# Kernel tuning notes

Measured on AMD Instinct MI355X. Metric: run time of the kernel, lower is better.

The kernel has to match this reference:

```python
import jax, jax.numpy as jnp
import numpy as np
from jax import lax

B, C, H = 64, 3, 224
F = 8  # number of 3x3 filters
POOL = (H - 2) // 2  # 111
FEAT = POOL * POOL * F  # 98568


def setup_inputs() -> dict:
    key = jax.random.key(0)
    ks = jax.random.split(key, 8)
    return {
        "x": jax.random.normal(ks[0], (B, C, H, H), dtype=jnp.float32),
        "filters": jax.random.normal(ks[1], (F, 3, 3), dtype=jnp.float32),
        "W1": jax.random.normal(ks[2], (FEAT, 512), dtype=jnp.float32) * 0.01,
        "b1": jax.random.normal(ks[3], (512,), dtype=jnp.float32) * 0.01,
        "W2": jax.random.normal(ks[4], (512, 256), dtype=jnp.float32) * 0.02,
        "b2": jax.random.normal(ks[5], (256,), dtype=jnp.float32) * 0.02,
        "Wo": jax.random.normal(ks[6], (256, 1000), dtype=jnp.float32) * 0.02,
        "bo": jax.random.normal(ks[7], (1000,), dtype=jnp.float32) * 0.02,
    }


def reference(x, filters, W1, b1, W2, b2, Wo, bo):
    # conv_r + conv_g + conv_b == conv(r+g+b, filt) by linearity -> sum channels once
    s = x.sum(axis=1, keepdims=True)  # [B,1,H,H]
    k = filters[:, None, :, :]  # [F,1,3,3] (OIHW)
    conv = lax.conv_general_dilated(
        s, k, window_strides=(1, 1), padding="VALID",
        dimension_numbers=("NCHW", "OIHW", "NCHW"))  # [B,F,222,222]
    conv = jax.nn.relu(conv)
    pooled = lax.reduce_window(
        conv, -jnp.inf, lax.max,
        window_dimensions=(1, 1, 2, 2), window_strides=(1, 1, 2, 2),
        padding="VALID")  # [B,F,111,111]
    flat = pooled.reshape(x.shape[0], -1)  # filter-major layout matches torch cat order
    h = jax.nn.relu(flat @ W1 + b1)
    h = jax.nn.relu(h @ W2 + b2)
    return jax.nn.softmax(h @ Wo + bo, axis=1)
```

## Files before the change

### kernel.cpp

```cpp
#include <hip/hip_runtime.h>
#include <math.h>

#define Bsz 64
#define Himg 224
#define HS (Himg*Himg)
#define PW 111
#define PP (PW*PW)
#define Fn 8
#define FEAT (Fn*PP)
#define FEATP 98592
#define KC 32
#define NT32_TOT 3081
#define NCH 192
#define N1 512
#define N2 256
#define N3 1000
#define RG 8

typedef short short8 __attribute__((ext_vector_type(8)));
typedef float f32x4 __attribute__((ext_vector_type(4)));

#define GLOAD_LDS16(g, l)                                                     \
  __builtin_amdgcn_global_load_lds(                                           \
      (const __attribute__((address_space(1))) void*)(g),                     \
      (__attribute__((address_space(3))) void*)(l), 16, 0, 0)

__device__ __forceinline__ void cvt_hilo(const float* v, short8& hi, short8& lo) {
#pragma unroll
  for (int j = 0; j < 8; j++) {
    unsigned u = __builtin_bit_cast(unsigned, v[j]);
    hi[j] = (short)(u >> 16);
    float hf = __builtin_bit_cast(float, u & 0xFFFF0000u);
    float r = v[j] - hf;
    lo[j] = (short)(__builtin_bit_cast(unsigned, r) >> 16);
  }
}

__device__ __forceinline__ unsigned packhl(float f) {
  unsigned u = __builtin_bit_cast(unsigned, f);
  unsigned hi = u >> 16;
  float hf = __builtin_bit_cast(float, u & 0xFFFF0000u);
  float r = f - hf;
  unsigned lo = __builtin_bit_cast(unsigned, r) >> 16;
  return (hi << 16) | (lo & 0xFFFFu);
}

__device__ __forceinline__ uint4 pack4(float4 f) {
  uint4 o;
  o.x = packhl(f.x); o.y = packhl(f.y); o.z = packhl(f.z); o.w = packhl(f.w);
  return o;
}

__global__ void k_convpool(const float* __restrict__ x, const float* __restrict__ filt,
                           float* __restrict__ flat) {
  int i = blockIdx.x * 256 + threadIdx.x;
  if (i < Bsz * (FEATP - FEAT))
    flat[(size_t)(i / 24) * FEATP + FEAT + (i % 24)] = 0.f;
  if (i >= Bsz * PP) return;
  int b = i / PP, r = i - b * PP;
  int py = r / PW, px = r - py * PW;
  const float* xb = x + (size_t)b * 3 * HS + (size_t)(2 * py) * Himg + 2 * px;
  float p[4][4];
#pragma unroll
  for (int dy = 0; dy < 4; dy++) {
    const float* row = xb + dy * Himg;
    float2 a0 = *(const float2*)(row);
    float2 a1 = *(const float2*)(row + 2);
    float2 b0 = *(const float2*)(row + HS);
    float2 b1 = *(const float2*)(row + HS + 2);
    float2 c0 = *(const float2*)(row + 2 * HS);
    float2 c1 = *(const float2*)(row + 2 * HS + 2);
    p[dy][0] = a0.x + b0.x + c0.x;
    p[dy][1] = a0.y + b0.y + c0.y;
    p[dy][2] = a1.x + b1.x + c1.x;
    p[dy][3] = a1.y + b1.y + c1.y;
  }
  float* outb = flat + (size_t)b * FEATP + r;
#pragma unroll
  for (int f = 0; f < Fn; f++) {
    float mx = 0.f;
#pragma unroll
    for (int oy = 0; oy < 2; oy++)
#pragma unroll
      for (int ox = 0; ox < 2; ox++) {
        float c = 0.f;
#pragma unroll
        for (int dy = 0; dy < 3; dy++)
#pragma unroll
          for (int dx = 0; dx < 3; dx++)
            c = fmaf(p[oy + dy][ox + dx], filt[f * 9 + dy * 3 + dx], c);
        mx = fmaxf(mx, c);
      }
    outb[(size_t)f * PP] = mx;
  }
}

__global__ void __launch_bounds__(256) k_gemm1(const float* __restrict__ A,
                                               const float* __restrict__ W,
                                               float* __restrict__ partial) {
  __shared__ float Wl[2][KC][128];
  __shared__ unsigned As[2][64 * 32];
  const int t = threadIdx.x;
  const int wv = t >> 6;
  const int lane = t & 63;
  const int wgid = blockIdx.x;
  const int nid = (wgid & 7) * 96 + (wgid >> 3);
  const int col0b = (nid & 3) * 128;
  const int c = nid >> 2;
  const int tile0 = c * 16 + min(c, 9);
  const int nt = (c < 9) ? 17 : 16;
  const int lrow = lane & 15;
  const int lg8 = (lane >> 4) * 8;
  const int gr = lg8 >> 2;
  const int sr = wv * 16 + (lane >> 3);
  const int sq = lane & 7;
  const int sgs = ((sq ^ (sr & 7)) << 2);
  const float* Ast = A + (size_t)sr * FEATP + sq * 4;
  const int wsr = lane >> 5;
  const int wscx = ((lane & 31) * 4) ^ ((wv & 1) << 4);
  const int wcol = wv * 32 + lrow;
  const int wcolsw = wcol ^ (((lg8 >> 3) & 1) << 4);

  f32x4 acc[4][2];
#pragma unroll
  for (int mf = 0; mf < 4; mf++)
#pragma unroll
    for (int nf = 0; nf < 2; nf++)
#pragma unroll
      for (int r = 0; r < 4; r++) acc[mf][nf][r] = 0.f;

  float4 fa0, fa1;

#define STAGE_W(buf, kt)                                                      \
  {                                                                           \
    const int kb = (kt) * KC + wv * 8;                                        \
    _Pragma("unroll")                                                         \
    for (int p = 0; p < 4; p++) {                                             \
      int krow = kb + 2 * p + wsr;                                            \
      krow = krow < FEAT ? krow : FEAT - 1;       \
      GLOAD_LDS16(W + (size_t)krow * N1 + col0b + wscx,                       \
                  &Wl[buf][wv * 8 + 2 * p][0]);                               \
    }                                                                         \
  }

  auto loadA = [&](int kb) {
    fa0 = *(const float4*)(Ast + kb);
    fa1 = *(const float4*)(Ast + (size_t)8 * FEATP + kb);
  };
  auto writeA = [&](int buf) {
    *(uint4*)&As[buf][sr * 32 + sgs] = pack4(fa0);
    *(uint4*)&As[buf][(sr + 8) * 32 + sgs] = pack4(fa1);
  };

  STAGE_W(0, tile0)
  loadA(tile0 * KC);
  writeA(0);
  __syncthreads();

  for (int s = 0; s < nt; s++) {
    const int buf = s & 1;
    const bool more = (s + 1) < nt;
    if (more) {
      STAGE_W(buf ^ 1, tile0 + s + 1)
      loadA((tile0 + s + 1) * KC);
    }
    float bv0[8], bv1[8];
#pragma unroll
    for (int j = 0; j < 8; j++) {
      bv0[j] = Wl[buf][lg8 + j][wcolsw];
      bv1[j] = Wl[buf][lg8 + j][wcolsw ^ 16];
    }
    short8 bhi[2], blo[2];
    cvt_hilo(bv0, bhi[0], blo[0]);
    cvt_hilo(bv1, bhi[1], blo[1]);
#pragma unroll
    for (int mf = 0; mf < 4; mf++) {
      const int r = mf * 16 + lrow;
      const int key = (r & 7);
      unsigned au[8];
      *(uint4*)(au + 0) = *(const uint4*)&As[buf][r * 32 + ((gr ^ key) << 2)];
      *(uint4*)(au + 4) = *(const uint4*)&As[buf][r * 32 + (((gr + 1) ^ key) << 2)];
      short8 ahi, alo;
#pragma unroll
      for (int j = 0; j < 8; j++) {
        ahi[j] = (short)(au[j] >> 16);
        alo[j] = (short)(au[j] & 0xFFFFu);
      }
#pragma unroll
      for (int nf = 0; nf < 2; nf++) {
        acc[mf][nf] = __builtin_amdgcn_mfma_f32_16x16x32_bf16(ahi, bhi[nf], acc[mf][nf], 0, 0, 0);
        acc[mf][nf] = __builtin_amdgcn_mfma_f32_16x16x32_bf16(ahi, blo[nf], acc[mf][nf], 0, 0, 0);
        acc[mf][nf] = __builtin_amdgcn_mfma_f32_16x16x32_bf16(alo, bhi[nf], acc[mf][nf], 0, 0, 0);
      }
    }
    if (more) writeA(buf ^ 1);
    __syncthreads();
  }

  const int drow = (lane >> 4) * 4;
#pragma unroll
  for (int mf = 0; mf < 4; mf++) {
#pragma unroll
    for (int nf = 0; nf < 2; nf++) {
      float* pp = partial + ((size_t)c * Bsz + mf * 16 + drow) * N1 +
                  col0b + wv * 32 + nf * 16 + lrow;
#pragma unroll
      for (int r = 0; r < 4; r++) pp[(size_t)r * N1] = acc[mf][nf][r];
    }
  }
}

__global__ void k_red1a(const float4* __restrict__ partial, float4* __restrict__ partial2) {
  int i = blockIdx.x * 256 + threadIdx.x;
  int g = blockIdx.y;
  int c0 = g * 24;
  const int Q = Bsz * N1 / 4;
  float4 s = make_float4(0.f, 0.f, 0.f, 0.f);
#pragma unroll 4
  for (int c = c0; c < c0 + 24; c++) {
    float4 v = partial[(size_t)c * Q + i];
    s.x += v.x; s.y += v.y; s.z += v.z; s.w += v.w;
  }
  partial2[(size_t)g * Q + i] = s;
}

__global__ void __launch_bounds__(256) k_gemm2(const float* __restrict__ partial2,
                                               const float* __restrict__ b1,
                                               const float* __restrict__ W2,
                                               const float* __restrict__ b2,
                                               float* __restrict__ h2) {
  const int m = blockIdx.x >> 2;
  const int nq = blockIdx.x & 3;
  const int t = threadIdx.x;
  __shared__ float a[N1];
  __shared__ float red[4][64];
#pragma unroll
  for (int e = 0; e < 2; e++) {
    int idx = e * 256 + t;
    float sum = 0.f;
#pragma unroll
    for (int g = 0; g < RG; g++)
      sum += partial2[(size_t)g * Bsz * N1 + (size_t)m * N1 + idx];
    a[idx] = fmaxf(sum + b1[idx], 0.f);
  }
  __syncthreads();
  const int col = nq * 64 + (t & 63);
  const int ks = (t >> 6) * 128;
  float sum = 0.f;
#pragma unroll 8
  for (int k = 0; k < 128; k++)
    sum = fmaf(a[ks + k], W2[(size_t)(ks + k) * N2 + col], sum);
  red[t >> 6][t & 63] = sum;
  __syncthreads();
  if (t < 64) {
    float tot = red[0][t] + red[1][t] + red[2][t] + red[3][t] + b2[nq * 64 + t];
    h2[(size_t)m * N2 + nq * 64 + t] = fmaxf(tot, 0.f);
  }
}

__global__ void __launch_bounds__(256) k_logits(const float* __restrict__ h2,
                                                const float* __restrict__ Wo,
                                                const float* __restrict__ bo,
                                                float* __restrict__ logits) {
  const int m = blockIdx.x >> 2;
  const int nc = blockIdx.x & 3;
  const int t = threadIdx.x;
  __shared__ float a[N2];
  a[t] = h2[(size_t)m * N2 + t];
  __syncthreads();
  const int col = nc * 250 + t;
  if (t >= 250) return;
  float sum = bo[col];
#pragma unroll 8
  for (int k = 0; k < N2; k++)
    sum = fmaf(a[k], Wo[(size_t)k * N3 + col], sum);
  logits[(size_t)m * N3 + col] = sum;
}

__global__ void __launch_bounds__(256) k_softmax(const float* __restrict__ logits,
                                                 float* __restrict__ out) {
  const int m = blockIdx.x;
  const int t = threadIdx.x;
  __shared__ float red[8];
  float vals[4];
  float vmax = -3.4e38f;
#pragma unroll
  for (int j = 0; j < 4; j++) {
    int n = j * 256 + t;
    vals[j] = (n < N3) ? logits[(size_t)m * N3 + n] : -3.4e38f;
    vmax = fmaxf(vmax, vals[j]);
  }
#pragma unroll
  for (int off = 32; off > 0; off >>= 1) vmax = fmaxf(vmax, __shfl_xor(vmax, off));
  const int wid = t >> 6;
  if ((t & 63) == 0) red[wid] = vmax;
  __syncthreads();
  vmax = fmaxf(fmaxf(red[0], red[1]), fmaxf(red[2], red[3]));
  float ev[4];
  float esum = 0.f;
#pragma unroll
  for (int j = 0; j < 4; j++) {
    int n = j * 256 + t;
    float e = (n < N3) ? __expf(vals[j] - vmax) : 0.f;
    ev[j] = e;
    esum += e;
  }
#pragma unroll
  for (int off = 32; off > 0; off >>= 1) esum += __shfl_xor(esum, off);
  if ((t & 63) == 0) red[4 + wid] = esum;
  __syncthreads();
  esum = red[4] + red[5] + red[6] + red[7];
  float inv = 1.f / esum;
#pragma unroll
  for (int j = 0; j < 4; j++) {
    int n = j * 256 + t;
    if (n < N3) out[(size_t)m * N3 + n] = ev[j] * inv;
  }
}

extern "C" void kernel_launch(void* const* d_in, const int* in_sizes, int n_in,
                              void* d_out, int out_size, void* d_ws, size_t ws_size,
                              hipStream_t stream) {
  const float* x = (const float*)d_in[0];
  const float* filters = (const float*)d_in[1];
  const float* W1 = (const float*)d_in[2];
  const float* b1 = (const float*)d_in[3];
  const float* W2 = (const float*)d_in[4];
  const float* b2 = (const float*)d_in[5];
  const float* Wo = (const float*)d_in[6];
  const float* bo = (const float*)d_in[7];
  float* out = (float*)d_out;

  float* ws = (float*)d_ws;
  float* flat = ws;
  float* partial = flat + (size_t)Bsz * FEATP;
  float* partial2 = partial + (size_t)NCH * Bsz * N1;
  float* h2 = partial2 + (size_t)RG * Bsz * N1;
  float* logits = h2 + (size_t)Bsz * N2;

  k_convpool<<<(Bsz * PP + 255) / 256, 256, 0, stream>>>(x, filters, flat);
  k_gemm1<<<4 * NCH, 256, 0, stream>>>(flat, W1, partial);
  dim3 gr(Bsz * N1 / 4 / 256, RG);
  k_red1a<<<gr, 256, 0, stream>>>((const float4*)partial, (float4*)partial2);
  k_gemm2<<<Bsz * 4, 256, 0, stream>>>(partial2, b1, W2, b2, h2);
  k_logits<<<Bsz * 4, 256, 0, stream>>>(h2, Wo, bo, logits);
  k_softmax<<<Bsz, 256, 0, stream>>>(logits, out);
}
```

Before: 89.74 us.

## Precompute bf16 hi/lo split in conv kernel and DMA A tiles into LDS

```diff
diff --git a/kernel.cpp b/kernel.cpp
--- a/kernel.cpp
+++ b/kernel.cpp
@@ -36,26 +36,13 @@
   }
 }
 
-__device__ __forceinline__ unsigned packhl(float f) {
-  unsigned u = __builtin_bit_cast(unsigned, f);
-  unsigned hi = u >> 16;
-  float hf = __builtin_bit_cast(float, u & 0xFFFF0000u);
-  float r = f - hf;
-  unsigned lo = __builtin_bit_cast(unsigned, r) >> 16;
-  return (hi << 16) | (lo & 0xFFFFu);
-}
-
-__device__ __forceinline__ uint4 pack4(float4 f) {
-  uint4 o;
-  o.x = packhl(f.x); o.y = packhl(f.y); o.z = packhl(f.z); o.w = packhl(f.w);
-  return o;
-}
-
 __global__ void k_convpool(const float* __restrict__ x, const float* __restrict__ filt,
-                           float* __restrict__ flat) {
+                           short* __restrict__ Ah, short* __restrict__ Al) {
   int i = blockIdx.x * 256 + threadIdx.x;
-  if (i < Bsz * (FEATP - FEAT))
-    flat[(size_t)(i / 24) * FEATP + FEAT + (i % 24)] = 0.f;
+  if (i < Bsz * (FEATP - FEAT)) {
+    size_t pidx = (size_t)(i / 24) * FEATP + FEAT + (i % 24);
+    Ah[pidx] = 0; Al[pidx] = 0;
+  }
   if (i >= Bsz * PP) return;
   int b = i / PP, r = i - b * PP;
   int py = r / PW, px = r - py * PW;
@@ -75,7 +62,7 @@
     p[dy][2] = a1.x + b1.x + c1.x;
     p[dy][3] = a1.y + b1.y + c1.y;
   }
-  float* outb = flat + (size_t)b * FEATP + r;
+  size_t base = (size_t)b * FEATP + r;
 #pragma unroll
   for (int f = 0; f < Fn; f++) {
     float mx = 0.f;
@@ -91,15 +78,21 @@
             c = fmaf(p[oy + dy][ox + dx], filt[f * 9 + dy * 3 + dx], c);
         mx = fmaxf(mx, c);
       }
-    outb[(size_t)f * PP] = mx;
-  }
-}
-
-__global__ void __launch_bounds__(256) k_gemm1(const float* __restrict__ A,
+    unsigned u = __builtin_bit_cast(unsigned, mx);
+    float hf = __builtin_bit_cast(float, u & 0xFFFF0000u);
+    float rr = mx - hf;
+    Ah[base + (size_t)f * PP] = (short)(u >> 16);
+    Al[base + (size_t)f * PP] = (short)(__builtin_bit_cast(unsigned, rr) >> 16);
+  }
+}
+
+__global__ void __launch_bounds__(256) k_gemm1(const short* __restrict__ Ah,
+                                               const short* __restrict__ Al,
                                                const float* __restrict__ W,
                                                float* __restrict__ partial) {
   __shared__ float Wl[2][KC][128];
-  __shared__ unsigned As[2][64 * 32];
+  __shared__ short Ashi[2][64 * 32];
+  __shared__ short Aslo[2][64 * 32];
   const int t = threadIdx.x;
   const int wv = t >> 6;
   const int lane = t & 63;
@@ -111,15 +104,11 @@
   const int nt = (c < 9) ? 17 : 16;
   const int lrow = lane & 15;
   const int lg8 = (lane >> 4) * 8;
-  const int gr = lg8 >> 2;
-  const int sr = wv * 16 + (lane >> 3);
-  const int sq = lane & 7;
-  const int sgs = ((sq ^ (sr & 7)) << 2);
-  const float* Ast = A + (size_t)sr * FEATP + sq * 4;
   const int wsr = lane >> 5;
   const int wscx = ((lane & 31) * 4) ^ ((wv & 1) << 4);
   const int wcol = wv * 32 + lrow;
   const int wcolsw = wcol ^ (((lg8 >> 3) & 1) << 4);
+  const size_t aoff = (size_t)(wv * 16 + (lane >> 2)) * FEATP + (lane & 3) * 8;
 
   f32x4 acc[4][2];
 #pragma unroll
@@ -128,8 +117,6 @@
     for (int nf = 0; nf < 2; nf++)
 #pragma unroll
       for (int r = 0; r < 4; r++) acc[mf][nf][r] = 0.f;
-
-  float4 fa0, fa1;
 
 #define STAGE_W(buf, kt)                                                      \
   {                                                                           \
@@ -142,19 +129,15 @@
                   &Wl[buf][wv * 8 + 2 * p][0]);                               \
     }                                                                         \
   }
-
-  auto loadA = [&](int kb) {
-    fa0 = *(const float4*)(Ast + kb);
-    fa1 = *(const float4*)(Ast + (size_t)8 * FEATP + kb);
-  };
-  auto writeA = [&](int buf) {
-    *(uint4*)&As[buf][sr * 32 + sgs] = pack4(fa0);
-    *(uint4*)&As[buf][(sr + 8) * 32 + sgs] = pack4(fa1);
-  };
+#define STAGE_A(buf, kt)                                                      \
+  {                                                                           \
+    const int kb = (kt) * KC;                                                 \
+    GLOAD_LDS16(Ah + aoff + kb, &Ashi[buf][wv * 16 * 32]);                    \
+    GLOAD_LDS16(Al + aoff + kb, &Aslo[buf][wv * 16 * 32]);                    \
+  }
 
   STAGE_W(0, tile0)
-  loadA(tile0 * KC);
-  writeA(0);
+  STAGE_A(0, tile0)
   __syncthreads();
 
   for (int s = 0; s < nt; s++) {
@@ -162,7 +145,7 @@
     const bool more = (s + 1) < nt;
     if (more) {
       STAGE_W(buf ^ 1, tile0 + s + 1)
-      loadA((tile0 + s + 1) * KC);
+      STAGE_A(buf ^ 1, tile0 + s + 1)
     }
     float bv0[8], bv1[8];
 #pragma unroll
@@ -176,16 +159,8 @@
 #pragma unroll
     for (int mf = 0; mf < 4; mf++) {
       const int r = mf * 16 + lrow;
-      const int key = (r & 7);
-      unsigned au[8];
-      *(uint4*)(au + 0) = *(const uint4*)&As[buf][r * 32 + ((gr ^ key) << 2)];
-      *(uint4*)(au + 4) = *(const uint4*)&As[buf][r * 32 + (((gr + 1) ^ key) << 2)];
-      short8 ahi, alo;
-#pragma unroll
-      for (int j = 0; j < 8; j++) {
-        ahi[j] = (short)(au[j] >> 16);
-        alo[j] = (short)(au[j] & 0xFFFFu);
-      }
+      short8 ahi = *(const short8*)&Ashi[buf][r * 32 + lg8];
+      short8 alo = *(const short8*)&Aslo[buf][r * 32 + lg8];
 #pragma unroll
       for (int nf = 0; nf < 2; nf++) {
         acc[mf][nf] = __builtin_amdgcn_mfma_f32_16x16x32_bf16(ahi, bhi[nf], acc[mf][nf], 0, 0, 0);
@@ -193,7 +168,6 @@
         acc[mf][nf] = __builtin_amdgcn_mfma_f32_16x16x32_bf16(alo, bhi[nf], acc[mf][nf], 0, 0, 0);
       }
     }
-    if (more) writeA(buf ^ 1);
     __syncthreads();
   }
 
@@ -331,15 +305,15 @@
   const float* bo = (const float*)d_in[7];
   float* out = (float*)d_out;
 
-  float* ws = (float*)d_ws;
-  float* flat = ws;
-  float* partial = flat + (size_t)Bsz * FEATP;
+  short* Ah = (short*)d_ws;
+  short* Al = Ah + (size_t)Bsz * FEATP;
+  float* partial = (float*)(Al + (size_t)Bsz * FEATP);
   float* partial2 = partial + (size_t)NCH * Bsz * N1;
   float* h2 = partial2 + (size_t)RG * Bsz * N1;
   float* logits = h2 + (size_t)Bsz * N2;
 
-  k_convpool<<<(Bsz * PP + 255) / 256, 256, 0, stream>>>(x, filters, flat);
-  k_gemm1<<<4 * NCH, 256, 0, stream>>>(flat, W1, partial);
+  k_convpool<<<(Bsz * PP + 255) / 256, 256, 0, stream>>>(x, filters, Ah, Al);
+  k_gemm1<<<4 * NCH, 256, 0, stream>>>(Ah, Al, W1, partial);
   dim3 gr(Bsz * N1 / 4 / 256, RG);
   k_red1a<<<gr, 256, 0, stream>>>((const float4*)partial, (float4*)partial2);
   k_gemm2<<<Bsz * 4, 256, 0, stream>>>(partial2, b1, W2, b2, h2);
```

Result: slower. 93.87 us (+4.6%).
